# Performance work log

Hardware: AMD Instinct MI355X
Metric: run time of the kernel (lower is better)

Reference implementation:

```python
import jax, jax.numpy as jnp
import numpy as np
import math

D_MODEL = 1024
D_STATE = 16
D_CONV = 4
EXPAND = 2
D_INNER = EXPAND * D_MODEL
DT_RANK = math.ceil(D_MODEL / 16)
EPS = 1e-5


def setup_inputs() -> dict:
    key = jax.random.key(0)
    ks = jax.random.split(key, 8)
    B, L = 2, 1024
    s = 0.02
    return {
        "hidden_states": jax.random.normal(ks[0], (B, L, D_MODEL), jnp.float32),
        "norm_weight": jnp.ones((D_MODEL,), jnp.float32),
        "in_proj_w": (jax.random.normal(ks[1], (2 * D_INNER, D_MODEL), jnp.float32) * s),
        "conv_w": (jax.random.normal(ks[2], (D_INNER, D_CONV), jnp.float32) * s),
        "conv_b": jnp.zeros((D_INNER,), jnp.float32),
        "x_proj_w": (jax.random.normal(ks[3], (DT_RANK + 2 * D_STATE, D_INNER), jnp.float32) * s),
        "dt_proj_w": (jax.random.normal(ks[4], (D_INNER, DT_RANK), jnp.float32) * s),
        "dt_proj_b": jax.random.uniform(ks[5], (D_INNER,), jnp.float32, -4.0, -2.0),
        "A_log": jnp.log(jnp.broadcast_to(jnp.arange(1, D_STATE + 1, dtype=jnp.float32), (D_INNER, D_STATE))),
        "D": jnp.ones((D_INNER,), jnp.float32),
        "out_proj_w": (jax.random.normal(ks[6], (D_MODEL, D_INNER), jnp.float32) * s),
    }


def _rmsnorm(x, w):
    # Faithful to source: rms = ||x||_2 / sqrt(d); x / (rms + eps) * w
    norm = jnp.linalg.norm(x, axis=-1, keepdims=True)
    rms = norm * (1.0 / math.sqrt(x.shape[-1]))
    return w * (x / (rms + EPS))


def _mamba(h, in_proj_w, conv_w, conv_b, x_proj_w, dt_proj_w, dt_proj_b, A_log, D, out_proj_w):
    B, L, _ = h.shape
    xz = h @ in_proj_w.T                      # (B,L,2*D_INNER)
    x, z = jnp.split(xz, 2, axis=-1)          # each (B,L,D_INNER)

    # causal depthwise conv1d along L, kernel D_CONV
    xpad = jnp.pad(x, ((0, 0), (D_CONV - 1, 0), (0, 0)))
    xc = conv_b
    for k in range(D_CONV):                   # tiny fixed loop over kernel taps
        xc = xc + xpad[:, k:k + L, :] * conv_w[:, k]
    xc = jax.nn.silu(xc)                      # (B,L,D_INNER)

    x_dbl = xc @ x_proj_w.T                   # (B,L,DT_RANK+2N)
    dt, Bm, Cm = jnp.split(x_dbl, [DT_RANK, DT_RANK + D_STATE], axis=-1)
    dt = jax.nn.softplus(dt @ dt_proj_w.T + dt_proj_b)   # (B,L,D_INNER)

    A = -jnp.exp(A_log)                       # (D_INNER,N)
    deltaA = jnp.exp(dt[..., None] * A)                      # (B,L,D_INNER,N)
    deltaBu = (dt * xc)[..., None] * Bm[:, :, None, :]        # (B,L,D_INNER,N)

    def step(hst, inp):
        dA, dBu, Ct = inp
        hst = dA * hst + dBu                  # (B,D_INNER,N)
        y = jnp.einsum('bdn,bn->bd', hst, Ct)
        return hst, y

    h0 = jnp.zeros((B, D_INNER, D_STATE), xc.dtype)
    _, ys = jax.lax.scan(step, h0, (deltaA.swapaxes(0, 1), deltaBu.swapaxes(0, 1), Cm.swapaxes(0, 1)))
    y = ys.swapaxes(0, 1)                     # (B,L,D_INNER)
    y = y + D * xc
    y = y * jax.nn.silu(z)
    return y @ out_proj_w.T                   # (B,L,D_MODEL)


def reference(hidden_states, norm_weight, in_proj_w, conv_w, conv_b, x_proj_w,
              dt_proj_w, dt_proj_b, A_log, D, out_proj_w):
    residual = hidden_states
    h = _rmsnorm(residual, norm_weight)
    out = _mamba(h, in_proj_w, conv_w, conv_b, x_proj_w, dt_proj_w, dt_proj_b,
                 A_log, D, out_proj_w)
    return out, residual
```

## Files before the change

kernel.cpp:

```cpp
#include <hip/hip_runtime.h>

typedef __bf16 bf16x8 __attribute__((ext_vector_type(8)));
typedef float f32x4 __attribute__((ext_vector_type(4)));

__device__ __forceinline__ float b2f(ushort u) {
    union { unsigned int i; float f; } v;
    v.i = ((unsigned int)u) << 16;
    return v.f;
}
__device__ __forceinline__ ushort f2b(float f) {
    union { float f; unsigned int i; } v;
    v.f = f;
    unsigned int x = v.i;
    unsigned int r = (x + 0x7fffu + ((x >> 16) & 1u)) >> 16;
    return (ushort)r;
}

#define D_MODEL 1024
#define D_INNER 2048
#define D_STATE 16
#define DT_RANK 64
#define NTOK    2048
#define LSEQ    1024
#define NCH     32
#define LC      32
#define KSL     16

__global__ __launch_bounds__(256) void cvt_all_kernel(
    const float* __restrict__ inproj, const float* __restrict__ outproj,
    const float* __restrict__ xprojw, const float* __restrict__ dtw,
    ushort* __restrict__ wIn, ushort* __restrict__ wOut,
    ushort* __restrict__ xpw, ushort* __restrict__ dtwb)
{
    int i = blockIdx.x * 256 + threadIdx.x;
    const float* src; ushort* dst; int off;
    if (i < 1048576)      { src = inproj;  dst = wIn;  off = i; }
    else if (i < 1572864) { src = outproj; dst = wOut; off = i - 1048576; }
    else if (i < 1622016) { src = xprojw;  dst = xpw;  off = i - 1572864; }
    else if (i < 1654784) { src = dtw;     dst = dtwb; off = i - 1622016; }
    else return;
    float4 v = *(const float4*)(src + (size_t)off * 4);
    ushort4 o;
    o.x = f2b(v.x); o.y = f2b(v.y); o.z = f2b(v.z); o.w = f2b(v.w);
    *(ushort4*)(dst + (size_t)off * 4) = o;
}

__global__ __launch_bounds__(256) void rmsnorm_kernel(
    const float* __restrict__ hs, const float* __restrict__ w,
    ushort* __restrict__ hout, float* __restrict__ resid)
{
    int t = blockIdx.x;
    int tid = threadIdx.x;
    float4 r4 = *(const float4*)(hs + (size_t)t * D_MODEL + tid * 4);
    float s = r4.x * r4.x + r4.y * r4.y + r4.z * r4.z + r4.w * r4.w;
    #pragma unroll
    for (int off = 32; off >= 1; off >>= 1) s += __shfl_xor(s, off);
    __shared__ float red[4];
    int lane = tid & 63, wid = tid >> 6;
    if (lane == 0) red[wid] = s;
    __syncthreads();
    float tot = red[0] + red[1] + red[2] + red[3];
    float inv = 1.0f / (sqrtf(tot) * (1.0f / 32.0f) + 1e-5f);
    float4 w4 = *(const float4*)(w + tid * 4);
    ushort4 o;
    o.x = f2b(w4.x * r4.x * inv);
    o.y = f2b(w4.y * r4.y * inv);
    o.z = f2b(w4.z * r4.z * inv);
    o.w = f2b(w4.w * r4.w * inv);
    *(ushort4*)(hout + (size_t)t * D_MODEL + tid * 4) = o;
    *(float4*)(resid + (size_t)t * D_MODEL + tid * 4) = r4;
}

__global__ __launch_bounds__(256) void gemm_xz_kernel(
    const ushort* __restrict__ Ag, const ushort* __restrict__ Wg,
    ushort* __restrict__ xq, ushort* __restrict__ zq, int K)
{
    __shared__ __align__(16) ushort sA[128 * 40];
    __shared__ __align__(16) ushort sB[128 * 40];
    int tid = threadIdx.x;
    int bm = blockIdx.x, bn = blockIdx.y;
    int wid = tid >> 6, lane = tid & 63;
    int wm = (wid >> 1) * 64, wn = (wid & 1) * 64;
    int l16 = lane & 15, q = lane >> 4;

    f32x4 acc[4][4];
    #pragma unroll
    for (int i = 0; i < 4; i++)
        #pragma unroll
        for (int j = 0; j < 4; j++)
            acc[i][j] = (f32x4){0.f, 0.f, 0.f, 0.f};

    const ushort* Abase = Ag + (size_t)bm * 128 * K;
    const ushort* Wbase = Wg + (size_t)bn * 128 * K;

    int r0 = tid >> 2, c0 = (tid & 3) << 3;
    const ushort* pA0 = Abase + (size_t)r0 * K + c0;
    const ushort* pA1 = Abase + (size_t)(r0 + 64) * K + c0;
    const ushort* pB0 = Wbase + (size_t)r0 * K + c0;
    const ushort* pB1 = Wbase + (size_t)(r0 + 64) * K + c0;

    uint4 pa0 = *(const uint4*)(pA0), pa1 = *(const uint4*)(pA1);
    uint4 pb0 = *(const uint4*)(pB0), pb1 = *(const uint4*)(pB1);

    for (int k0 = 0; k0 < K; k0 += 32) {
        *(uint4*)(sA + r0 * 40 + c0)        = pa0;
        *(uint4*)(sA + (r0 + 64) * 40 + c0) = pa1;
        *(uint4*)(sB + r0 * 40 + c0)        = pb0;
        *(uint4*)(sB + (r0 + 64) * 40 + c0) = pb1;
        __syncthreads();
        if (k0 + 32 < K) {
            pa0 = *(const uint4*)(pA0 + k0 + 32);
            pa1 = *(const uint4*)(pA1 + k0 + 32);
            pb0 = *(const uint4*)(pB0 + k0 + 32);
            pb1 = *(const uint4*)(pB1 + k0 + 32);
        }
        bf16x8 af[4], bfr[4];
        #pragma unroll
        for (int i = 0; i < 4; i++)
            af[i] = *(const bf16x8*)(sA + (wm + i * 16 + l16) * 40 + q * 8);
        #pragma unroll
        for (int j = 0; j < 4; j++)
            bfr[j] = *(const bf16x8*)(sB + (wn + j * 16 + l16) * 40 + q * 8);
        #pragma unroll
        for (int i = 0; i < 4; i++)
            #pragma unroll
            for (int j = 0; j < 4; j++)
                acc[i][j] = __builtin_amdgcn_mfma_f32_16x16x32_bf16(af[i], bfr[j], acc[i][j], 0, 0, 0);
        __syncthreads();
    }

    ushort* dst = (bn < 16) ? xq : zq;
    int row0 = bm * 128 + wm + q * 4;
    int col0 = (bn & 15) * 128 + wn + l16;
    #pragma unroll
    for (int i = 0; i < 4; i++)
        #pragma unroll
        for (int j = 0; j < 4; j++)
            #pragma unroll
            for (int r = 0; r < 4; r++)
                dst[(size_t)(row0 + i * 16 + r) * D_INNER + col0 + j * 16] =
                    f2b(acc[i][j][r]);
}

__global__ __launch_bounds__(256) void gemm64_kernel(
    const ushort* __restrict__ Ag, const ushort* __restrict__ Wg,
    float* __restrict__ Cf, int M, int N, int K)
{
    __shared__ __align__(16) ushort sA[64 * 72];
    __shared__ __align__(16) ushort sB[64 * 72];
    int tid = threadIdx.x;
    int bm = blockIdx.x, bn = blockIdx.y;
    int wid = tid >> 6, lane = tid & 63;
    int wm = wid * 16;
    int l16 = lane & 15, q = lane >> 4;

    f32x4 acc[4];
    #pragma unroll
    for (int j = 0; j < 4; j++) acc[j] = (f32x4){0.f, 0.f, 0.f, 0.f};

    const ushort* Abase = Ag + (size_t)bm * 64 * K;
    const ushort* Wbase = Wg + (size_t)bn * 64 * K;

    int r0 = tid >> 3, c0 = (tid & 7) << 3;
    const ushort* pA0 = Abase + (size_t)r0 * K + c0;
    const ushort* pA1 = Abase + (size_t)(r0 + 32) * K + c0;
    const ushort* pB0 = Wbase + (size_t)r0 * K + c0;
    const ushort* pB1 = Wbase + (size_t)(r0 + 32) * K + c0;

    uint4 pa0 = *(const uint4*)(pA0), pa1 = *(const uint4*)(pA1);
    uint4 pb0 = *(const uint4*)(pB0), pb1 = *(const uint4*)(pB1);

    for (int k0 = 0; k0 < K; k0 += 64) {
        *(uint4*)(sA + r0 * 72 + c0)        = pa0;
        *(uint4*)(sA + (r0 + 32) * 72 + c0) = pa1;
        *(uint4*)(sB + r0 * 72 + c0)        = pb0;
        *(uint4*)(sB + (r0 + 32) * 72 + c0) = pb1;
        __syncthreads();
        if (k0 + 64 < K) {
            pa0 = *(const uint4*)(pA0 + k0 + 64);
            pa1 = *(const uint4*)(pA1 + k0 + 64);
            pb0 = *(const uint4*)(pB0 + k0 + 64);
            pb1 = *(const uint4*)(pB1 + k0 + 64);
        }
        #pragma unroll
        for (int ks = 0; ks < 2; ks++) {
            bf16x8 af = *(const bf16x8*)(sA + (wm + l16) * 72 + ks * 32 + q * 8);
            bf16x8 bfr[4];
            #pragma unroll
            for (int j = 0; j < 4; j++)
                bfr[j] = *(const bf16x8*)(sB + (j * 16 + l16) * 72 + ks * 32 + q * 8);
            #pragma unroll
            for (int j = 0; j < 4; j++)
                acc[j] = __builtin_amdgcn_mfma_f32_16x16x32_bf16(af, bfr[j], acc[j], 0, 0, 0);
        }
        __syncthreads();
    }

    int row0 = bm * 64 + wm + q * 4;
    int col0 = bn * 64 + l16;
    #pragma unroll
    for (int j = 0; j < 4; j++)
        #pragma unroll
        for (int r = 0; r < 4; r++)
            Cf[(size_t)(row0 + r) * N + col0 + j * 16] = acc[j][r];
}

__global__ __launch_bounds__(256) void conv_silu_kernel(
    const ushort* __restrict__ xq, const float* __restrict__ cw,
    const float* __restrict__ cb, ushort* __restrict__ xcb)
{
    int idx = blockIdx.x * 256 + threadIdx.x;
    int d = idx & (D_INNER - 1);
    int t = idx >> 11;
    int l = t & (LSEQ - 1), b = t >> 10;
    float4 w4 = *(const float4*)(cw + d * 4);
    float acc = cb[d];
    float wk[4] = {w4.x, w4.y, w4.z, w4.w};
    #pragma unroll
    for (int k = 0; k < 4; k++) {
        int ll = l - 3 + k;
        float xv = (ll >= 0) ? b2f(xq[(((size_t)(b * LSEQ + ll)) << 11) + d]) : 0.f;
        acc += xv * wk[k];
    }
    float sg = acc / (1.f + __expf(-acc));
    xcb[idx] = f2b(sg);
}

__global__ __launch_bounds__(256) void xproj_partial_kernel(
    const ushort* __restrict__ xcb, const ushort* __restrict__ wq,
    float* __restrict__ partials)
{
    __shared__ __align__(16) ushort sA[128 * 32];
    __shared__ __align__(16) ushort sB[96 * 32];
    int tid = threadIdx.x;
    int bm = blockIdx.x, sl = blockIdx.y;
    int wid = tid >> 6, lane = tid & 63;
    int wm = wid * 32;
    int l16 = lane & 15, q = lane >> 4;

    f32x4 acc[2][6];
    #pragma unroll
    for (int i = 0; i < 2; i++)
        #pragma unroll
        for (int j = 0; j < 6; j++)
            acc[i][j] = (f32x4){0.f, 0.f, 0.f, 0.f};

    const ushort* Abase = xcb + (size_t)bm * 128 * D_INNER;
    int kbase = sl * (D_INNER / KSL);

    for (int kk = 0; kk < D_INNER / KSL; kk += 32) {
        int k0 = kbase + kk;
        __syncthreads();
        #pragma unroll
        for (int i = tid; i < 512; i += 256) {
            int r = i >> 2, c = (i & 3) << 3;
            *(uint4*)(sA + i * 8) = *(const uint4*)(Abase + (size_t)r * D_INNER + k0 + c);
        }
        for (int i = tid; i < 384; i += 256) {
            int r = i >> 2, c = (i & 3) << 3;
            *(uint4*)(sB + i * 8) = *(const uint4*)(wq + (size_t)r * D_INNER + k0 + c);
        }
        __syncthreads();
        bf16x8 af[2], bfr[6];
        #pragma unroll
        for (int i = 0; i < 2; i++)
            af[i] = *(const bf16x8*)(sA + (wm + i * 16 + l16) * 32 + q * 8);
        #pragma unroll
        for (int j = 0; j < 6; j++)
            bfr[j] = *(const bf16x8*)(sB + (j * 16 + l16) * 32 + q * 8);
        #pragma unroll
        for (int i = 0; i < 2; i++)
            #pragma unroll
            for (int j = 0; j < 6; j++)
                acc[i][j] = __builtin_amdgcn_mfma_f32_16x16x32_bf16(af[i], bfr[j], acc[i][j], 0, 0, 0);
    }

    float* out = partials + (size_t)sl * NTOK * 96;
    int row0 = bm * 128 + wm + q * 4;
    #pragma unroll
    for (int i = 0; i < 2; i++)
        #pragma unroll
        for (int j = 0; j < 6; j++)
            #pragma unroll
            for (int r = 0; r < 4; r++)
                out[(size_t)(row0 + i * 16 + r) * 96 + j * 16 + l16] = acc[i][j][r];
}

__global__ __launch_bounds__(256) void xproj_reduce_kernel(
    const float* __restrict__ partials, float* __restrict__ xdbl,
    ushort* __restrict__ xdbl64)
{
    int idx = blockIdx.x * 256 + threadIdx.x;
    float s = 0.f;
    #pragma unroll
    for (int sl = 0; sl < KSL; sl++)
        s += partials[(size_t)sl * NTOK * 96 + idx];
    xdbl[idx] = s;
    int col = idx % 96;
    if (col < DT_RANK)
        xdbl64[(size_t)(idx / 96) * DT_RANK + col] = f2b(s);
}

__global__ __launch_bounds__(256) void dt_gemm_kernel(
    const ushort* __restrict__ xd64, const ushort* __restrict__ dtwq,
    const float* __restrict__ dtb, ushort* __restrict__ dtout)
{
    __shared__ __align__(16) ushort sA[64 * 72];
    __shared__ __align__(16) ushort sB[64 * 72];
    int tid = threadIdx.x;
    int bm = blockIdx.x, bn = blockIdx.y;
    int wid = tid >> 6, lane = tid & 63;
    int wm = wid * 16;
    int l16 = lane & 15, q = lane >> 4;

    const ushort* Abase = xd64 + (size_t)bm * 64 * DT_RANK;
    const ushort* Bbase = dtwq + (size_t)bn * 64 * DT_RANK;
    #pragma unroll
    for (int i = tid; i < 512; i += 256) {
        int r = i >> 3, c = (i & 7) << 3;
        *(uint4*)(sA + r * 72 + c) = *(const uint4*)(Abase + (size_t)r * DT_RANK + c);
        *(uint4*)(sB + r * 72 + c) = *(const uint4*)(Bbase + (size_t)r * DT_RANK + c);
    }
    __syncthreads();

    f32x4 acc[4];
    #pragma unroll
    for (int j = 0; j < 4; j++) acc[j] = (f32x4){0.f, 0.f, 0.f, 0.f};

    #pragma unroll
    for (int ks = 0; ks < 2; ks++) {
        bf16x8 af = *(const bf16x8*)(sA + (wm + l16) * 72 + ks * 32 + q * 8);
        bf16x8 bfr[4];
        #pragma unroll
        for (int j = 0; j < 4; j++)
            bfr[j] = *(const bf16x8*)(sB + (j * 16 + l16) * 72 + ks * 32 + q * 8);
        #pragma unroll
        for (int j = 0; j < 4; j++)
            acc[j] = __builtin_amdgcn_mfma_f32_16x16x32_bf16(af, bfr[j], acc[j], 0, 0, 0);
    }

    __syncthreads();
    #pragma unroll
    for (int j = 0; j < 4; j++) {
        float bias = dtb[bn * 64 + j * 16 + l16];
        #pragma unroll
        for (int r = 0; r < 4; r++) {
            float s = acc[j][r] + bias;
            float sp = (s > 20.f) ? s : log1pf(__expf(s));
            sA[(wm + q * 4 + r) * 72 + j * 16 + l16] = f2b(sp);
        }
    }
    __syncthreads();
    int row0 = bm * 64, col0 = bn * 64;
    #pragma unroll
    for (int rep = 0; rep < 2; rep++) {
        int off = rep * 2048 + tid * 8;
        int row = off >> 6, col = off & 63;
        *(uint4*)(dtout + (size_t)(row0 + row) * D_INNER + col0 + col) =
            *(const uint4*)(sA + row * 72 + col);
    }
}

__global__ __launch_bounds__(256) void scan_partA_kernel(
    const ushort* __restrict__ dt, const ushort* __restrict__ xcq,
    const float* __restrict__ xdbl, const float* __restrict__ Alog,
    float2* __restrict__ ch1, float2* __restrict__ ch2)
{
    __shared__ float sBC[LC][32];
    int bid = blockIdx.x;
    int g = bid & 7;
    int c = (bid >> 3) & (NCH - 1);
    int b = bid >> 8;
    int tid = threadIdx.x;
    int lane = tid & 63, wid = tid >> 6;
    int d = g * 256 + wid * 64 + lane;
    int l0 = c * LC;

    {
        int r = tid >> 3, c4 = (tid & 7) * 4;
        *(float4*)&sBC[r][c4] =
            *(const float4*)(xdbl + ((size_t)(b * LSEQ + l0 + r)) * 96 + 64 + c4);
    }
    float A[16];
    #pragma unroll
    for (int k = 0; k < 4; k++)
        *(float4*)&A[k * 4] = *(const float4*)(Alog + d * D_STATE + k * 4);
    #pragma unroll
    for (int n = 0; n < 16; n++) A[n] = -__expf(A[n]);
    __syncthreads();

    const ushort* dtp = dt  + ((size_t)(b * LSEQ + l0)) * D_INNER + d;
    const ushort* xcp = xcq + ((size_t)(b * LSEQ + l0)) * D_INNER + d;

    float h[16], ap[16];
    #pragma unroll
    for (int n = 0; n < 16; n++) { h[n] = 0.f; ap[n] = 1.f; }

    for (int l = 0; l < LC; l++) {
        float dtv = b2f(dtp[(size_t)l * D_INNER]);
        float xcv = b2f(xcp[(size_t)l * D_INNER]);
        float t = dtv * xcv;
        float Bv[16];
        #pragma unroll
        for (int k = 0; k < 4; k++)
            *(float4*)&Bv[k * 4] = *(const float4*)&sBC[l][k * 4];
        #pragma unroll
        for (int n = 0; n < 16; n++) {
            float a = __expf(dtv * A[n]);
            h[n] = h[n] * a + t * Bv[n];
            ap[n] *= a;
        }
    }

    float2* outp = (c < 16 ? ch1 : ch2) +
                   ((size_t)((b * 16 + (c & 15)) * D_INNER + d)) * D_STATE;
    #pragma unroll
    for (int n = 0; n < 16; n += 2) {
        float4 v = {ap[n], h[n], ap[n + 1], h[n + 1]};
        *(float4*)&outp[n] = v;
    }
}

__global__ __launch_bounds__(256) void scan_partB_kernel(
    float2* __restrict__ ch1, float2* __restrict__ ch2)
{
    int kk = blockIdx.x * 256 + threadIdx.x;
    int b = kk >> 15, dn = kk & 32767;
    float run = 0.f;
    #pragma unroll
    for (int c = 0; c < NCH; c++) {
        float2* p = (c < 16 ? ch1 : ch2) +
                    (size_t)(b * 16 + (c & 15)) * 32768 + dn;
        float2 v = *p;
        p->x = run;
        run = v.x * run + v.y;
    }
}

__global__ __launch_bounds__(256) void scan_partC_kernel(
    const ushort* __restrict__ dt, const ushort* __restrict__ xcq,
    const float* __restrict__ xdbl, const ushort* __restrict__ zq,
    const float* __restrict__ Alog, const float* __restrict__ Dp,
    const float2* __restrict__ ch1, const float2* __restrict__ ch2,
    ushort* __restrict__ yg)
{
    __shared__ float sBC[LC][32];
    int bid = blockIdx.x;
    int g = bid & 7;
    int c = (bid >> 3) & (NCH - 1);
    int b = bid >> 8;
    int tid = threadIdx.x;
    int lane = tid & 63, wid = tid >> 6;
    int d = g * 256 + wid * 64 + lane;
    int l0 = c * LC;

    {
        int r = tid >> 3, c4 = (tid & 7) * 4;
        *(float4*)&sBC[r][c4] =
            *(const float4*)(xdbl + ((size_t)(b * LSEQ + l0 + r)) * 96 + 64 + c4);
    }
    float A[16];
    #pragma unroll
    for (int k = 0; k < 4; k++)
        *(float4*)&A[k * 4] = *(const float4*)(Alog + d * D_STATE + k * 4);
    #pragma unroll
    for (int n = 0; n < 16; n++) A[n] = -__expf(A[n]);
    float Dd = Dp[d];

    const float2* hip_ = (c < 16 ? ch1 : ch2) +
                         ((size_t)((b * 16 + (c & 15)) * D_INNER + d)) * D_STATE;
    float h[16];
    #pragma unroll
    for (int n = 0; n < 16; n += 2) {
        float4 v = *(const float4*)&hip_[n];
        h[n] = v.x; h[n + 1] = v.z;
    }
    __syncthreads();

    const ushort* dtp = dt  + ((size_t)(b * LSEQ + l0)) * D_INNER + d;
    const ushort* xcp = xcq + ((size_t)(b * LSEQ + l0)) * D_INNER + d;
    const ushort* zp  = zq  + ((size_t)(b * LSEQ + l0)) * D_INNER + d;
    ushort* yp = yg + ((size_t)(b * LSEQ + l0)) * D_INNER + d;

    for (int l = 0; l < LC; l++) {
        float dtv = b2f(dtp[(size_t)l * D_INNER]);
        float xcv = b2f(xcp[(size_t)l * D_INNER]);
        float zv  = b2f(zp[(size_t)l * D_INNER]);
        float t = dtv * xcv;
        float Bv[16], Cv[16];
        #pragma unroll
        for (int k = 0; k < 4; k++) {
            *(float4*)&Bv[k * 4] = *(const float4*)&sBC[l][k * 4];
            *(float4*)&Cv[k * 4] = *(const float4*)&sBC[l][16 + k * 4];
        }
        float p0 = 0.f, p1 = 0.f, p2 = 0.f, p3 = 0.f;
        #pragma unroll
        for (int n = 0; n < 16; n += 4) {
            float a0 = __expf(dtv * A[n]);
            float a1 = __expf(dtv * A[n + 1]);
            float a2 = __expf(dtv * A[n + 2]);
            float a3 = __expf(dtv * A[n + 3]);
            h[n]     = h[n] * a0 + t * Bv[n];
            h[n + 1] = h[n + 1] * a1 + t * Bv[n + 1];
            h[n + 2] = h[n + 2] * a2 + t * Bv[n + 2];
            h[n + 3] = h[n + 3] * a3 + t * Bv[n + 3];
            p0 += h[n] * Cv[n];
            p1 += h[n + 1] * Cv[n + 1];
            p2 += h[n + 2] * Cv[n + 2];
            p3 += h[n + 3] * Cv[n + 3];
        }
        float p = (p0 + p1) + (p2 + p3);
        float y = p + Dd * xcv;
        float sz = zv / (1.f + __expf(-zv));
        yp[(size_t)l * D_INNER] = f2b(y * sz);
    }
}

extern "C" void kernel_launch(void* const* d_in, const int* in_sizes, int n_in,
                              void* d_out, int out_size, void* d_ws, size_t ws_size,
                              hipStream_t stream)
{
    const float* hs      = (const float*)d_in[0];
    const float* norm_w  = (const float*)d_in[1];
    const float* inproj  = (const float*)d_in[2];
    const float* convw   = (const float*)d_in[3];
    const float* convb   = (const float*)d_in[4];
    const float* xprojw  = (const float*)d_in[5];
    const float* dtw     = (const float*)d_in[6];
    const float* dtb     = (const float*)d_in[7];
    const float* alog    = (const float*)d_in[8];
    const float* dvec    = (const float*)d_in[9];
    const float* outproj = (const float*)d_in[10];

    float* out_main  = (float*)d_out;
    float* out_resid = (float*)d_out + (size_t)NTOK * D_MODEL;

    char* ws = (char*)d_ws;
    ushort* xq      = (ushort*)(ws);
    ushort* zq      = (ushort*)(ws +  9437184);
    ushort* xcb     = (ushort*)(ws + 18874368);
    ushort* dtq     = (ushort*)(ws + 28311552);
    float2* ch1     = (float2*)(ws + 37748736);
    float2* ch2     = (float2*)(ws + 47185920);
    float*  xdbl    = (float*) (ws + 56623104);
    ushort* xd64    = (ushort*)(ws + 57671680);
    ushort* xpw_b   = (ushort*)(ws + 58195968);
    ushort* dtw_b   = (ushort*)(ws + 58720256);
    ushort* wIn     = (ushort*)(ws + 59768832);
    ushort* wOut    = (ushort*)(ws + 69206016);
    ushort* h_bf16  = (ushort*)(ws + 74448896);
    ushort* yg_bf16 = (ushort*)(ws + 18874368);
    float*  xprojP  = (float*) (ws + 79691776);

    yg_bf16 = (ushort*)(ws + 79691776);

    cvt_all_kernel<<<6464, 256, 0, stream>>>(
        inproj, outproj, xprojw, dtw, wIn, wOut, xpw_b, dtw_b);

    rmsnorm_kernel<<<NTOK, 256, 0, stream>>>(hs, norm_w, h_bf16, out_resid);

    gemm_xz_kernel<<<dim3(NTOK / 128, (2 * D_INNER) / 128), 256, 0, stream>>>(
        h_bf16, wIn, xq, zq, D_MODEL);

    conv_silu_kernel<<<(NTOK * D_INNER) / 256, 256, 0, stream>>>(
        xq, convw, convb, xcb);

    xproj_partial_kernel<<<dim3(NTOK / 128, KSL), 256, 0, stream>>>(
        xcb, xpw_b, xprojP);
    xproj_reduce_kernel<<<NTOK * 96 / 256, 256, 0, stream>>>(xprojP, xdbl, xd64);

    dt_gemm_kernel<<<dim3(NTOK / 64, D_INNER / 64), 256, 0, stream>>>(
        xd64, dtw_b, dtb, dtq);

    scan_partA_kernel<<<512, 256, 0, stream>>>(dtq, xcb, xdbl, alog, ch1, ch2);
    scan_partB_kernel<<<256, 256, 0, stream>>>(ch1, ch2);
    scan_partC_kernel<<<512, 256, 0, stream>>>(dtq, xcb, xdbl, zq,
                                               alog, dvec, ch1, ch2, yg_bf16);

    gemm64_kernel<<<dim3(NTOK / 64, D_MODEL / 64), 256, 0, stream>>>(
        yg_bf16, wOut, out_main, NTOK, D_MODEL, D_INNER);
}
```

Before: 265.1 us.

## Fuse causal conv+SiLU into x-proj and scan kernels, merge prep kernels

Removes the standalone conv_silu kernel and its materialized xc buffer. The depthwise causal conv and SiLU are now recomputed from xq inside the x-projection tile loader and inside both scan passes, with the scans carrying a rolling three-tap history. The weight-conversion and RMSNorm kernels are also merged into one launch. This saves a full write and reread of the 2048x2048 bf16 intermediate plus two launches, at the cost of redundant conv math and extra shifted loads in the GEMM loader and scans.

Result: no change. 266.5 us (+0.5%).

```diff
diff --git a/kernel.cpp b/kernel.cpp
--- a/kernel.cpp
+++ b/kernel.cpp
@@ -26,49 +26,49 @@
 #define LC      32
 #define KSL     16
 
-__global__ __launch_bounds__(256) void cvt_all_kernel(
+__global__ __launch_bounds__(256) void prep_kernel(
+    const float* __restrict__ hs, const float* __restrict__ w,
+    ushort* __restrict__ hout, float* __restrict__ resid,
     const float* __restrict__ inproj, const float* __restrict__ outproj,
     const float* __restrict__ xprojw, const float* __restrict__ dtw,
     ushort* __restrict__ wIn, ushort* __restrict__ wOut,
     ushort* __restrict__ xpw, ushort* __restrict__ dtwb)
 {
-    int i = blockIdx.x * 256 + threadIdx.x;
-    const float* src; ushort* dst; int off;
-    if (i < 1048576)      { src = inproj;  dst = wIn;  off = i; }
-    else if (i < 1572864) { src = outproj; dst = wOut; off = i - 1048576; }
-    else if (i < 1622016) { src = xprojw;  dst = xpw;  off = i - 1572864; }
-    else if (i < 1654784) { src = dtw;     dst = dtwb; off = i - 1622016; }
-    else return;
-    float4 v = *(const float4*)(src + (size_t)off * 4);
-    ushort4 o;
-    o.x = f2b(v.x); o.y = f2b(v.y); o.z = f2b(v.z); o.w = f2b(v.w);
-    *(ushort4*)(dst + (size_t)off * 4) = o;
-}
-
-__global__ __launch_bounds__(256) void rmsnorm_kernel(
-    const float* __restrict__ hs, const float* __restrict__ w,
-    ushort* __restrict__ hout, float* __restrict__ resid)
-{
-    int t = blockIdx.x;
+    int blk = blockIdx.x;
     int tid = threadIdx.x;
-    float4 r4 = *(const float4*)(hs + (size_t)t * D_MODEL + tid * 4);
-    float s = r4.x * r4.x + r4.y * r4.y + r4.z * r4.z + r4.w * r4.w;
-    #pragma unroll
-    for (int off = 32; off >= 1; off >>= 1) s += __shfl_xor(s, off);
-    __shared__ float red[4];
-    int lane = tid & 63, wid = tid >> 6;
-    if (lane == 0) red[wid] = s;
-    __syncthreads();
-    float tot = red[0] + red[1] + red[2] + red[3];
-    float inv = 1.0f / (sqrtf(tot) * (1.0f / 32.0f) + 1e-5f);
-    float4 w4 = *(const float4*)(w + tid * 4);
-    ushort4 o;
-    o.x = f2b(w4.x * r4.x * inv);
-    o.y = f2b(w4.y * r4.y * inv);
-    o.z = f2b(w4.z * r4.z * inv);
-    o.w = f2b(w4.w * r4.w * inv);
-    *(ushort4*)(hout + (size_t)t * D_MODEL + tid * 4) = o;
-    *(float4*)(resid + (size_t)t * D_MODEL + tid * 4) = r4;
+    if (blk < NTOK) {
+        int t = blk;
+        float4 r4 = *(const float4*)(hs + (size_t)t * D_MODEL + tid * 4);
+        float s = r4.x * r4.x + r4.y * r4.y + r4.z * r4.z + r4.w * r4.w;
+        #pragma unroll
+        for (int off = 32; off >= 1; off >>= 1) s += __shfl_xor(s, off);
+        __shared__ float red[4];
+        int lane = tid & 63, wid = tid >> 6;
+        if (lane == 0) red[wid] = s;
+        __syncthreads();
+        float tot = red[0] + red[1] + red[2] + red[3];
+        float inv = 1.0f / (sqrtf(tot) * (1.0f / 32.0f) + 1e-5f);
+        float4 w4 = *(const float4*)(w + tid * 4);
+        ushort4 o;
+        o.x = f2b(w4.x * r4.x * inv);
+        o.y = f2b(w4.y * r4.y * inv);
+        o.z = f2b(w4.z * r4.z * inv);
+        o.w = f2b(w4.w * r4.w * inv);
+        *(ushort4*)(hout + (size_t)t * D_MODEL + tid * 4) = o;
+        *(float4*)(resid + (size_t)t * D_MODEL + tid * 4) = r4;
+    } else {
+        int i = (blk - NTOK) * 256 + tid;
+        const float* src; ushort* dst; int off;
+        if (i < 1048576)      { src = inproj;  dst = wIn;  off = i; }
+        else if (i < 1572864) { src = outproj; dst = wOut; off = i - 1048576; }
+        else if (i < 1622016) { src = xprojw;  dst = xpw;  off = i - 1572864; }
+        else if (i < 1654784) { src = dtw;     dst = dtwb; off = i - 1622016; }
+        else return;
+        float4 v = *(const float4*)(src + (size_t)off * 4);
+        ushort4 o;
+        o.x = f2b(v.x); o.y = f2b(v.y); o.z = f2b(v.z); o.w = f2b(v.w);
+        *(ushort4*)(dst + (size_t)off * 4) = o;
+    }
 }
 
 __global__ __launch_bounds__(256) void gemm_xz_kernel(
@@ -205,29 +205,9 @@
             Cf[(size_t)(row0 + r) * N + col0 + j * 16] = acc[j][r];
 }
 
-__global__ __launch_bounds__(256) void conv_silu_kernel(
+__global__ __launch_bounds__(256) void xproj_partial_kernel(
     const ushort* __restrict__ xq, const float* __restrict__ cw,
-    const float* __restrict__ cb, ushort* __restrict__ xcb)
-{
-    int idx = blockIdx.x * 256 + threadIdx.x;
-    int d = idx & (D_INNER - 1);
-    int t = idx >> 11;
-    int l = t & (LSEQ - 1), b = t >> 10;
-    float4 w4 = *(const float4*)(cw + d * 4);
-    float acc = cb[d];
-    float wk[4] = {w4.x, w4.y, w4.z, w4.w};
-    #pragma unroll
-    for (int k = 0; k < 4; k++) {
-        int ll = l - 3 + k;
-        float xv = (ll >= 0) ? b2f(xq[(((size_t)(b * LSEQ + ll)) << 11) + d]) : 0.f;
-        acc += xv * wk[k];
-    }
-    float sg = acc / (1.f + __expf(-acc));
-    xcb[idx] = f2b(sg);
-}
-
-__global__ __launch_bounds__(256) void xproj_partial_kernel(
-    const ushort* __restrict__ xcb, const ushort* __restrict__ wq,
+    const float* __restrict__ cb, const ushort* __restrict__ wq,
     float* __restrict__ partials)
 {
     __shared__ __align__(16) ushort sA[128 * 32];
@@ -245,16 +225,36 @@
         for (int j = 0; j < 6; j++)
             acc[i][j] = (f32x4){0.f, 0.f, 0.f, 0.f};
 
-    const ushort* Abase = xcb + (size_t)bm * 128 * D_INNER;
     int kbase = sl * (D_INNER / KSL);
+    const uint4 zero4 = {0u, 0u, 0u, 0u};
 
     for (int kk = 0; kk < D_INNER / KSL; kk += 32) {
         int k0 = kbase + kk;
         __syncthreads();
         #pragma unroll
         for (int i = tid; i < 512; i += 256) {
-            int r = i >> 2, c = (i & 3) << 3;
-            *(uint4*)(sA + i * 8) = *(const uint4*)(Abase + (size_t)r * D_INNER + k0 + c);
+            int r = i >> 2, c8 = (i & 3) << 3;
+            int tok = bm * 128 + r;
+            int l = tok & (LSEQ - 1);
+            const ushort* xp = xq + (size_t)tok * D_INNER + k0 + c8;
+            uint4 x3 = (l >= 3) ? *(const uint4*)(xp - 3 * D_INNER) : zero4;
+            uint4 x2 = (l >= 2) ? *(const uint4*)(xp - 2 * D_INNER) : zero4;
+            uint4 x1 = (l >= 1) ? *(const uint4*)(xp - 1 * D_INNER) : zero4;
+            uint4 x0 = *(const uint4*)(xp);
+            const ushort* t3 = (const ushort*)&x3;
+            const ushort* t2 = (const ushort*)&x2;
+            const ushort* t1 = (const ushort*)&x1;
+            const ushort* t0 = (const ushort*)&x0;
+            ushort outv[8];
+            #pragma unroll
+            for (int jj = 0; jj < 8; jj++) {
+                int d = k0 + c8 + jj;
+                float4 w4 = *(const float4*)(cw + d * 4);
+                float a = cb[d] + b2f(t3[jj]) * w4.x + b2f(t2[jj]) * w4.y
+                                + b2f(t1[jj]) * w4.z + b2f(t0[jj]) * w4.w;
+                outv[jj] = f2b(a / (1.f + __expf(-a)));
+            }
+            *(uint4*)(sA + i * 8) = *(const uint4*)outv;
         }
         for (int i = tid; i < 384; i += 256) {
             int r = i >> 2, c = (i & 3) << 3;
@@ -362,7 +362,8 @@
 }
 
 __global__ __launch_bounds__(256) void scan_partA_kernel(
-    const ushort* __restrict__ dt, const ushort* __restrict__ xcq,
+    const ushort* __restrict__ dt, const ushort* __restrict__ xq,
+    const float* __restrict__ cw, const float* __restrict__ cb,
     const float* __restrict__ xdbl, const float* __restrict__ Alog,
     float2* __restrict__ ch1, float2* __restrict__ ch2)
 {
@@ -387,10 +388,19 @@
         *(float4*)&A[k * 4] = *(const float4*)(Alog + d * D_STATE + k * 4);
     #pragma unroll
     for (int n = 0; n < 16; n++) A[n] = -__expf(A[n]);
+    float4 w4 = *(const float4*)(cw + d * 4);
+    float cbv = cb[d];
     __syncthreads();
 
-    const ushort* dtp = dt  + ((size_t)(b * LSEQ + l0)) * D_INNER + d;
-    const ushort* xcp = xcq + ((size_t)(b * LSEQ + l0)) * D_INNER + d;
+    const ushort* dtp = dt + ((size_t)(b * LSEQ + l0)) * D_INNER + d;
+    const ushort* xp  = xq + ((size_t)(b * LSEQ + l0)) * D_INNER + d;
+
+    float xm3 = 0.f, xm2 = 0.f, xm1 = 0.f;
+    if (c > 0) {
+        xm3 = b2f(xp[-3 * D_INNER]);
+        xm2 = b2f(xp[-2 * D_INNER]);
+        xm1 = b2f(xp[-1 * D_INNER]);
+    }
 
     float h[16], ap[16];
     #pragma unroll
@@ -398,7 +408,10 @@
 
     for (int l = 0; l < LC; l++) {
         float dtv = b2f(dtp[(size_t)l * D_INNER]);
-        float xcv = b2f(xcp[(size_t)l * D_INNER]);
+        float xcur = b2f(xp[(size_t)l * D_INNER]);
+        float cv = cbv + xm3 * w4.x + xm2 * w4.y + xm1 * w4.z + xcur * w4.w;
+        float xcv = cv / (1.f + __expf(-cv));
+        xm3 = xm2; xm2 = xm1; xm1 = xcur;
         float t = dtv * xcv;
         float Bv[16];
         #pragma unroll
@@ -438,7 +451,8 @@
 }
 
 __global__ __launch_bounds__(256) void scan_partC_kernel(
-    const ushort* __restrict__ dt, const ushort* __restrict__ xcq,
+    const ushort* __restrict__ dt, const ushort* __restrict__ xq,
+    const float* __restrict__ cw, const float* __restrict__ cb,
     const float* __restrict__ xdbl, const ushort* __restrict__ zq,
     const float* __restrict__ Alog, const float* __restrict__ Dp,
     const float2* __restrict__ ch1, const float2* __restrict__ ch2,
@@ -466,6 +480,8 @@
     #pragma unroll
     for (int n = 0; n < 16; n++) A[n] = -__expf(A[n]);
     float Dd = Dp[d];
+    float4 w4 = *(const float4*)(cw + d * 4);
+    float cbv = cb[d];
 
     const float2* hip_ = (c < 16 ? ch1 : ch2) +
                          ((size_t)((b * 16 + (c & 15)) * D_INNER + d)) * D_STATE;
@@ -477,15 +493,25 @@
     }
     __syncthreads();
 
-    const ushort* dtp = dt  + ((size_t)(b * LSEQ + l0)) * D_INNER + d;
-    const ushort* xcp = xcq + ((size_t)(b * LSEQ + l0)) * D_INNER + d;
-    const ushort* zp  = zq  + ((size_t)(b * LSEQ + l0)) * D_INNER + d;
+    const ushort* dtp = dt + ((size_t)(b * LSEQ + l0)) * D_INNER + d;
+    const ushort* xp  = xq + ((size_t)(b * LSEQ + l0)) * D_INNER + d;
+    const ushort* zp  = zq + ((size_t)(b * LSEQ + l0)) * D_INNER + d;
     ushort* yp = yg + ((size_t)(b * LSEQ + l0)) * D_INNER + d;
+
+    float xm3 = 0.f, xm2 = 0.f, xm1 = 0.f;
+    if (c > 0) {
+        xm3 = b2f(xp[-3 * D_INNER]);
+        xm2 = b2f(xp[-2 * D_INNER]);
+        xm1 = b2f(xp[-1 * D_INNER]);
+    }
 
     for (int l = 0; l < LC; l++) {
         float dtv = b2f(dtp[(size_t)l * D_INNER]);
-        float xcv = b2f(xcp[(size_t)l * D_INNER]);
+        float xcur = b2f(xp[(size_t)l * D_INNER]);
         float zv  = b2f(zp[(size_t)l * D_INNER]);
+        float cv = cbv + xm3 * w4.x + xm2 * w4.y + xm1 * w4.z + xcur * w4.w;
+        float xcv = cv / (1.f + __expf(-cv));
+        xm3 = xm2; xm2 = xm1; xm1 = xcur;
         float t = dtv * xcv;
         float Bv[16], Cv[16];
         #pragma unroll
@@ -538,43 +564,36 @@
     char* ws = (char*)d_ws;
     ushort* xq      = (ushort*)(ws);
     ushort* zq      = (ushort*)(ws +  9437184);
-    ushort* xcb     = (ushort*)(ws + 18874368);
-    ushort* dtq     = (ushort*)(ws + 28311552);
-    float2* ch1     = (float2*)(ws + 37748736);
-    float2* ch2     = (float2*)(ws + 47185920);
-    float*  xdbl    = (float*) (ws + 56623104);
-    ushort* xd64    = (ushort*)(ws + 57671680);
-    ushort* xpw_b   = (ushort*)(ws + 58195968);
-    ushort* dtw_b   = (ushort*)(ws + 58720256);
-    ushort* wIn     = (ushort*)(ws + 59768832);
-    ushort* wOut    = (ushort*)(ws + 69206016);
-    ushort* h_bf16  = (ushort*)(ws + 74448896);
-    ushort* yg_bf16 = (ushort*)(ws + 18874368);
-    float*  xprojP  = (float*) (ws + 79691776);
-
-    yg_bf16 = (ushort*)(ws + 79691776);
-
-    cvt_all_kernel<<<6464, 256, 0, stream>>>(
+    ushort* dtq     = (ushort*)(ws + 18874368);
+    float2* ch1     = (float2*)(ws + 28311552);
+    float2* ch2     = (float2*)(ws + 37748736);
+    float*  xdbl    = (float*) (ws + 47185920);
+    ushort* xd64    = (ushort*)(ws + 48234496);
+    ushort* xpw_b   = (ushort*)(ws + 48758784);
+    ushort* dtw_b   = (ushort*)(ws + 49283072);
+    ushort* wIn     = (ushort*)(ws + 50331648);
+    ushort* wOut    = (ushort*)(ws + 59768832);
+    ushort* h_bf16  = (ushort*)(ws + 65011712);
+    float*  xprojP  = (float*) (ws + 70254592);
+    ushort* yg_bf16 = (ushort*)(ws + 83886080);
+
+    prep_kernel<<<NTOK + 6464, 256, 0, stream>>>(
+        hs, norm_w, h_bf16, out_resid,
         inproj, outproj, xprojw, dtw, wIn, wOut, xpw_b, dtw_b);
-
-    rmsnorm_kernel<<<NTOK, 256, 0, stream>>>(hs, norm_w, h_bf16, out_resid);
 
     gemm_xz_kernel<<<dim3(NTOK / 128, (2 * D_INNER) / 128), 256, 0, stream>>>(
         h_bf16, wIn, xq, zq, D_MODEL);
 
-    conv_silu_kernel<<<(NTOK * D_INNER) / 256, 256, 0, stream>>>(
-        xq, convw, convb, xcb);
-
     xproj_partial_kernel<<<dim3(NTOK / 128, KSL), 256, 0, stream>>>(
-        xcb, xpw_b, xprojP);
+        xq, convw, convb, xpw_b, xprojP);
     xproj_reduce_kernel<<<NTOK * 96 / 256, 256, 0, stream>>>(xprojP, xdbl, xd64);
 
     dt_gemm_kernel<<<dim3(NTOK / 64, D_INNER / 64), 256, 0, stream>>>(
         xd64, dtw_b, dtb, dtq);
 
-    scan_partA_kernel<<<512, 256, 0, stream>>>(dtq, xcb, xdbl, alog, ch1, ch2);
+    scan_partA_kernel<<<512, 256, 0, stream>>>(dtq, xq, convw, convb, xdbl, alog, ch1, ch2);
     scan_partB_kernel<<<256, 256, 0, stream>>>(ch1, ch2);
-    scan_partC_kernel<<<512, 256, 0, stream>>>(dtq, xcb, xdbl, zq,
+    scan_partC_kernel<<<512, 256, 0, stream>>>(dtq, xq, convw, convb, xdbl, zq,
                                                alog, dvec, ch1, ch2, yg_bf16);
 
     gemm64_kernel<<<dim3(NTOK / 64, D_MODEL / 64), 256, 0, stream>>>(
```

## Use direct global-to-LDS loads with XOR swizzle in GEMMs and fuse prep kernels

Applied to the files above, without the earlier changes.

Both bf16 GEMM kernels now stage tiles with global_load_lds 16-byte direct loads into an unpadded, XOR-swizzled LDS layout instead of register-staged prefetch and padded stores. The xz GEMM's K step grows from 32 to 64. The rmsnorm and weight-conversion kernels are merged into one launch, and workspace offsets are rearranged. The goal is to cut VGPR staging and LDS bank conflicts and to save a launch, but the register prefetch overlap is lost because loads now sit between two barriers with no double buffering.

New measurement: 262.7 us. About the same (-0.9%).

```diff
diff --git a/kernel.cpp b/kernel.cpp
--- a/kernel.cpp
+++ b/kernel.cpp
@@ -14,6 +14,15 @@
     unsigned int x = v.i;
     unsigned int r = (x + 0x7fffu + ((x >> 16) & 1u)) >> 16;
     return (ushort)r;
+}
+__device__ __forceinline__ void gload16(const ushort* g, ushort* l) {
+    __builtin_amdgcn_global_load_lds(
+        (const __attribute__((address_space(1))) unsigned int*)g,
+        (__attribute__((address_space(3))) unsigned int*)l, 16, 0, 0);
+}
+__device__ __forceinline__ bf16x8 ldsfrag(const ushort* s, int row, int cq) {
+    int p = cq ^ (row & 7);
+    return *(const bf16x8*)(s + row * 64 + p * 8);
 }
 
 #define D_MODEL 1024
@@ -26,57 +35,57 @@
 #define LC      32
 #define KSL     16
 
-__global__ __launch_bounds__(256) void cvt_all_kernel(
+__global__ __launch_bounds__(256) void prep_kernel(
+    const float* __restrict__ hs, const float* __restrict__ w,
+    ushort* __restrict__ hout, float* __restrict__ resid,
     const float* __restrict__ inproj, const float* __restrict__ outproj,
     const float* __restrict__ xprojw, const float* __restrict__ dtw,
     ushort* __restrict__ wIn, ushort* __restrict__ wOut,
     ushort* __restrict__ xpw, ushort* __restrict__ dtwb)
 {
-    int i = blockIdx.x * 256 + threadIdx.x;
-    const float* src; ushort* dst; int off;
-    if (i < 1048576)      { src = inproj;  dst = wIn;  off = i; }
-    else if (i < 1572864) { src = outproj; dst = wOut; off = i - 1048576; }
-    else if (i < 1622016) { src = xprojw;  dst = xpw;  off = i - 1572864; }
-    else if (i < 1654784) { src = dtw;     dst = dtwb; off = i - 1622016; }
-    else return;
-    float4 v = *(const float4*)(src + (size_t)off * 4);
-    ushort4 o;
-    o.x = f2b(v.x); o.y = f2b(v.y); o.z = f2b(v.z); o.w = f2b(v.w);
-    *(ushort4*)(dst + (size_t)off * 4) = o;
-}
-
-__global__ __launch_bounds__(256) void rmsnorm_kernel(
-    const float* __restrict__ hs, const float* __restrict__ w,
-    ushort* __restrict__ hout, float* __restrict__ resid)
-{
-    int t = blockIdx.x;
-    int tid = threadIdx.x;
-    float4 r4 = *(const float4*)(hs + (size_t)t * D_MODEL + tid * 4);
-    float s = r4.x * r4.x + r4.y * r4.y + r4.z * r4.z + r4.w * r4.w;
-    #pragma unroll
-    for (int off = 32; off >= 1; off >>= 1) s += __shfl_xor(s, off);
-    __shared__ float red[4];
-    int lane = tid & 63, wid = tid >> 6;
-    if (lane == 0) red[wid] = s;
-    __syncthreads();
-    float tot = red[0] + red[1] + red[2] + red[3];
-    float inv = 1.0f / (sqrtf(tot) * (1.0f / 32.0f) + 1e-5f);
-    float4 w4 = *(const float4*)(w + tid * 4);
-    ushort4 o;
-    o.x = f2b(w4.x * r4.x * inv);
-    o.y = f2b(w4.y * r4.y * inv);
-    o.z = f2b(w4.z * r4.z * inv);
-    o.w = f2b(w4.w * r4.w * inv);
-    *(ushort4*)(hout + (size_t)t * D_MODEL + tid * 4) = o;
-    *(float4*)(resid + (size_t)t * D_MODEL + tid * 4) = r4;
+    int blk = blockIdx.x;
+    int tid = threadIdx.x;
+    if (blk < NTOK) {
+        int t = blk;
+        float4 r4 = *(const float4*)(hs + (size_t)t * D_MODEL + tid * 4);
+        float s = r4.x * r4.x + r4.y * r4.y + r4.z * r4.z + r4.w * r4.w;
+        #pragma unroll
+        for (int off = 32; off >= 1; off >>= 1) s += __shfl_xor(s, off);
+        __shared__ float red[4];
+        int lane = tid & 63, wid = tid >> 6;
+        if (lane == 0) red[wid] = s;
+        __syncthreads();
+        float tot = red[0] + red[1] + red[2] + red[3];
+        float inv = 1.0f / (sqrtf(tot) * (1.0f / 32.0f) + 1e-5f);
+        float4 w4 = *(const float4*)(w + tid * 4);
+        ushort4 o;
+        o.x = f2b(w4.x * r4.x * inv);
+        o.y = f2b(w4.y * r4.y * inv);
+        o.z = f2b(w4.z * r4.z * inv);
+        o.w = f2b(w4.w * r4.w * inv);
+        *(ushort4*)(hout + (size_t)t * D_MODEL + tid * 4) = o;
+        *(float4*)(resid + (size_t)t * D_MODEL + tid * 4) = r4;
+    } else {
+        int i = (blk - NTOK) * 256 + tid;
+        const float* src; ushort* dst; int off;
+        if (i < 1048576)      { src = inproj;  dst = wIn;  off = i; }
+        else if (i < 1572864) { src = outproj; dst = wOut; off = i - 1048576; }
+        else if (i < 1622016) { src = xprojw;  dst = xpw;  off = i - 1572864; }
+        else if (i < 1654784) { src = dtw;     dst = dtwb; off = i - 1622016; }
+        else return;
+        float4 v = *(const float4*)(src + (size_t)off * 4);
+        ushort4 o;
+        o.x = f2b(v.x); o.y = f2b(v.y); o.z = f2b(v.z); o.w = f2b(v.w);
+        *(ushort4*)(dst + (size_t)off * 4) = o;
+    }
 }
 
 __global__ __launch_bounds__(256) void gemm_xz_kernel(
     const ushort* __restrict__ Ag, const ushort* __restrict__ Wg,
     ushort* __restrict__ xq, ushort* __restrict__ zq, int K)
 {
-    __shared__ __align__(16) ushort sA[128 * 40];
-    __shared__ __align__(16) ushort sB[128 * 40];
+    __shared__ __align__(16) ushort sA[128 * 64];
+    __shared__ __align__(16) ushort sB[128 * 64];
     int tid = threadIdx.x;
     int bm = blockIdx.x, bn = blockIdx.y;
     int wid = tid >> 6, lane = tid & 63;
@@ -93,40 +102,41 @@
     const ushort* Abase = Ag + (size_t)bm * 128 * K;
     const ushort* Wbase = Wg + (size_t)bn * 128 * K;
 
-    int r0 = tid >> 2, c0 = (tid & 3) << 3;
-    const ushort* pA0 = Abase + (size_t)r0 * K + c0;
-    const ushort* pA1 = Abase + (size_t)(r0 + 64) * K + c0;
-    const ushort* pB0 = Wbase + (size_t)r0 * K + c0;
-    const ushort* pB1 = Wbase + (size_t)(r0 + 64) * K + c0;
-
-    uint4 pa0 = *(const uint4*)(pA0), pa1 = *(const uint4*)(pA1);
-    uint4 pb0 = *(const uint4*)(pB0), pb1 = *(const uint4*)(pB1);
-
-    for (int k0 = 0; k0 < K; k0 += 32) {
-        *(uint4*)(sA + r0 * 40 + c0)        = pa0;
-        *(uint4*)(sA + (r0 + 64) * 40 + c0) = pa1;
-        *(uint4*)(sB + r0 * 40 + c0)        = pb0;
-        *(uint4*)(sB + (r0 + 64) * 40 + c0) = pb1;
-        __syncthreads();
-        if (k0 + 32 < K) {
-            pa0 = *(const uint4*)(pA0 + k0 + 32);
-            pa1 = *(const uint4*)(pA1 + k0 + 32);
-            pb0 = *(const uint4*)(pB0 + k0 + 32);
-            pb1 = *(const uint4*)(pB1 + k0 + 32);
-        }
-        bf16x8 af[4], bfr[4];
-        #pragma unroll
-        for (int i = 0; i < 4; i++)
-            af[i] = *(const bf16x8*)(sA + (wm + i * 16 + l16) * 40 + q * 8);
-        #pragma unroll
-        for (int j = 0; j < 4; j++)
-            bfr[j] = *(const bf16x8*)(sB + (wn + j * 16 + l16) * 40 + q * 8);
-        #pragma unroll
-        for (int i = 0; i < 4; i++)
+    int segr = lane >> 3, segc = lane & 7;
+    size_t goff[4]; int sseg[4];
+    #pragma unroll
+    for (int t = 0; t < 4; t++) {
+        int s = wid * 4 + t;
+        int r = s * 8 + segr;
+        int gc = segc ^ (r & 7);
+        sseg[t] = s * 512;
+        goff[t] = (size_t)r * K + gc * 8;
+    }
+
+    for (int k0 = 0; k0 < K; k0 += 64) {
+        __syncthreads();
+        #pragma unroll
+        for (int t = 0; t < 4; t++) {
+            gload16(Abase + goff[t] + k0, sA + sseg[t]);
+            gload16(Wbase + goff[t] + k0, sB + sseg[t]);
+        }
+        __syncthreads();
+        #pragma unroll
+        for (int ks = 0; ks < 2; ks++) {
+            int cq = ks * 4 + q;
+            bf16x8 af[4], bfr[4];
+            #pragma unroll
+            for (int i = 0; i < 4; i++)
+                af[i] = ldsfrag(sA, wm + i * 16 + l16, cq);
             #pragma unroll
             for (int j = 0; j < 4; j++)
-                acc[i][j] = __builtin_amdgcn_mfma_f32_16x16x32_bf16(af[i], bfr[j], acc[i][j], 0, 0, 0);
-        __syncthreads();
+                bfr[j] = ldsfrag(sB, wn + j * 16 + l16, cq);
+            #pragma unroll
+            for (int i = 0; i < 4; i++)
+                #pragma unroll
+                for (int j = 0; j < 4; j++)
+                    acc[i][j] = __builtin_amdgcn_mfma_f32_16x16x32_bf16(af[i], bfr[j], acc[i][j], 0, 0, 0);
+        }
     }
 
     ushort* dst = (bn < 16) ? xq : zq;
@@ -146,8 +156,8 @@
     const ushort* __restrict__ Ag, const ushort* __restrict__ Wg,
     float* __restrict__ Cf, int M, int N, int K)
 {
-    __shared__ __align__(16) ushort sA[64 * 72];
-    __shared__ __align__(16) ushort sB[64 * 72];
+    __shared__ __align__(16) ushort sA[64 * 64];
+    __shared__ __align__(16) ushort sB[64 * 64];
     int tid = threadIdx.x;
     int bm = blockIdx.x, bn = blockIdx.y;
     int wid = tid >> 6, lane = tid & 63;
@@ -161,39 +171,37 @@
     const ushort* Abase = Ag + (size_t)bm * 64 * K;
     const ushort* Wbase = Wg + (size_t)bn * 64 * K;
 
-    int r0 = tid >> 3, c0 = (tid & 7) << 3;
-    const ushort* pA0 = Abase + (size_t)r0 * K + c0;
-    const ushort* pA1 = Abase + (size_t)(r0 + 32) * K + c0;
-    const ushort* pB0 = Wbase + (size_t)r0 * K + c0;
-    const ushort* pB1 = Wbase + (size_t)(r0 + 32) * K + c0;
-
-    uint4 pa0 = *(const uint4*)(pA0), pa1 = *(const uint4*)(pA1);
-    uint4 pb0 = *(const uint4*)(pB0), pb1 = *(const uint4*)(pB1);
+    int segr = lane >> 3, segc = lane & 7;
+    size_t goff[2]; int sseg[2];
+    #pragma unroll
+    for (int t = 0; t < 2; t++) {
+        int s = wid * 2 + t;
+        int r = s * 8 + segr;
+        int gc = segc ^ (r & 7);
+        sseg[t] = s * 512;
+        goff[t] = (size_t)r * K + gc * 8;
+    }
 
     for (int k0 = 0; k0 < K; k0 += 64) {
-        *(uint4*)(sA + r0 * 72 + c0)        = pa0;
-        *(uint4*)(sA + (r0 + 32) * 72 + c0) = pa1;
-        *(uint4*)(sB + r0 * 72 + c0)        = pb0;
-        *(uint4*)(sB + (r0 + 32) * 72 + c0) = pb1;
-        __syncthreads();
-        if (k0 + 64 < K) {
-            pa0 = *(const uint4*)(pA0 + k0 + 64);
-            pa1 = *(const uint4*)(pA1 + k0 + 64);
-            pb0 = *(const uint4*)(pB0 + k0 + 64);
-            pb1 = *(const uint4*)(pB1 + k0 + 64);
-        }
+        __syncthreads();
+        #pragma unroll
+        for (int t = 0; t < 2; t++) {
+            gload16(Abase + goff[t] + k0, sA + sseg[t]);
+            gload16(Wbase + goff[t] + k0, sB + sseg[t]);
+        }
+        __syncthreads();
         #pragma unroll
         for (int ks = 0; ks < 2; ks++) {
-            bf16x8 af = *(const bf16x8*)(sA + (wm + l16) * 72 + ks * 32 + q * 8);
+            int cq = ks * 4 + q;
+            bf16x8 af = ldsfrag(sA, wm + l16, cq);
             bf16x8 bfr[4];
             #pragma unroll
             for (int j = 0; j < 4; j++)
-                bfr[j] = *(const bf16x8*)(sB + (j * 16 + l16) * 72 + ks * 32 + q * 8);
+                bfr[j] = ldsfrag(sB, j * 16 + l16, cq);
             #pragma unroll
             for (int j = 0; j < 4; j++)
                 acc[j] = __builtin_amdgcn_mfma_f32_16x16x32_bf16(af, bfr[j], acc[j], 0, 0, 0);
         }
-        __syncthreads();
     }
 
     int row0 = bm * 64 + wm + q * 4;
@@ -538,26 +546,23 @@
     char* ws = (char*)d_ws;
     ushort* xq      = (ushort*)(ws);
     ushort* zq      = (ushort*)(ws +  9437184);
-    ushort* xcb     = (ushort*)(ws + 18874368);
-    ushort* dtq     = (ushort*)(ws + 28311552);
-    float2* ch1     = (float2*)(ws + 37748736);
-    float2* ch2     = (float2*)(ws + 47185920);
-    float*  xdbl    = (float*) (ws + 56623104);
-    ushort* xd64    = (ushort*)(ws + 57671680);
-    ushort* xpw_b   = (ushort*)(ws + 58195968);
-    ushort* dtw_b   = (ushort*)(ws + 58720256);
-    ushort* wIn     = (ushort*)(ws + 59768832);
-    ushort* wOut    = (ushort*)(ws + 69206016);
-    ushort* h_bf16  = (ushort*)(ws + 74448896);
-    ushort* yg_bf16 = (ushort*)(ws + 18874368);
-    float*  xprojP  = (float*) (ws + 79691776);
-
-    yg_bf16 = (ushort*)(ws + 79691776);
-
-    cvt_all_kernel<<<6464, 256, 0, stream>>>(
+    ushort* dtq     = (ushort*)(ws + 18874368);
+    float2* ch1     = (float2*)(ws + 28311552);
+    float2* ch2     = (float2*)(ws + 37748736);
+    float*  xdbl    = (float*) (ws + 47185920);
+    ushort* xd64    = (ushort*)(ws + 48234496);
+    ushort* xpw_b   = (ushort*)(ws + 48758784);
+    ushort* dtw_b   = (ushort*)(ws + 49283072);
+    ushort* wIn     = (ushort*)(ws + 50331648);
+    ushort* wOut    = (ushort*)(ws + 59768832);
+    ushort* h_bf16  = (ushort*)(ws + 65011712);
+    float*  xprojP  = (float*) (ws + 70254592);
+    ushort* yg_bf16 = (ushort*)(ws + 83886080);
+    ushort* xcb     = (ushort*)(ws + 92274688);
+
+    prep_kernel<<<NTOK + 6464, 256, 0, stream>>>(
+        hs, norm_w, h_bf16, out_resid,
         inproj, outproj, xprojw, dtw, wIn, wOut, xpw_b, dtw_b);
-
-    rmsnorm_kernel<<<NTOK, 256, 0, stream>>>(hs, norm_w, h_bf16, out_resid);
 
     gemm_xz_kernel<<<dim3(NTOK / 128, (2 * D_INNER) / 128), 256, 0, stream>>>(
         h_bf16, wIn, xq, zq, D_MODEL);
```
